# Kernel tuning notes

Measured on AMD Instinct MI355X. Metric: run time of the kernel, lower is better.

The kernel has to match this reference:

```python
import jax, jax.numpy as jnp
import numpy as np

# SREChead (single level, width=0.25): stem 1x1 (128->64) + two 3x3 convs (64->64),
# each Conv->BN(eval, folded into scale/shift)->SiLU, then 1x1 reg (4ch) and obj (1ch)
# heads, followed by YOLOX-style grid decode.
B, C_IN, HGT, WID = 64, 128, 80, 80
C_H = 64            # int(256 * 0.25)
STRIDE = 32


def _conv(x, w):
    # NCHW conv, stride 1, SAME padding (pad=(k-1)//2 as in BaseConv)
    return jax.lax.conv_general_dilated(
        x, w, window_strides=(1, 1), padding='SAME',
        dimension_numbers=('NCHW', 'OIHW', 'NCHW'))


def _bn_silu(y, scale, shift):
    # eval-mode BatchNorm folded to per-channel affine, then SiLU
    return jax.nn.silu(y * scale[None, :, None, None] + shift[None, :, None, None])


def setup_inputs() -> dict:
    key = jax.random.key(0)
    ks = jax.random.split(key, 12)

    def w(k, o, i, kh, kw, s=0.05):
        return jax.random.normal(k, (o, i, kh, kw), jnp.float32) * s

    def bn(k, c):
        k1, k2 = jax.random.split(k)
        scale = 1.0 + 0.1 * jax.random.normal(k1, (c,), jnp.float32)
        shift = 0.05 * jax.random.normal(k2, (c,), jnp.float32)
        return scale, shift

    stem_scale, stem_shift = bn(ks[2], C_H)
    c1_scale, c1_shift = bn(ks[4], C_H)
    c2_scale, c2_shift = bn(ks[6], C_H)
    return {
        'x': jax.random.normal(ks[0], (B, C_IN, HGT, WID), jnp.float32),
        'stem_w': w(ks[1], C_H, C_IN, 1, 1),
        'stem_scale': stem_scale, 'stem_shift': stem_shift,
        'c1_w': w(ks[3], C_H, C_H, 3, 3),
        'c1_scale': c1_scale, 'c1_shift': c1_shift,
        'c2_w': w(ks[5], C_H, C_H, 3, 3),
        'c2_scale': c2_scale, 'c2_shift': c2_shift,
        'reg_w': w(ks[7], 4, C_H, 1, 1),
        'reg_b': jnp.zeros((4,), jnp.float32),
        'obj_w': w(ks[8], 1, C_H, 1, 1),
        'obj_b': jnp.zeros((1,), jnp.float32),
    }


def reference(x, stem_w, stem_scale, stem_shift,
              c1_w, c1_scale, c1_shift,
              c2_w, c2_scale, c2_shift,
              reg_w, reg_b, obj_w, obj_b):
    f = _bn_silu(_conv(x, stem_w), stem_scale, stem_shift)       # [B,64,H,W]
    f = _bn_silu(_conv(f, c1_w), c1_scale, c1_shift)
    f = _bn_silu(_conv(f, c2_w), c2_scale, c2_shift)
    reg = _conv(f, reg_w) + reg_b[None, :, None, None]           # [B,4,H,W]
    obj = jax.nn.sigmoid(_conv(f, obj_w) + obj_b[None, :, None, None])  # [B,1,H,W]
    out = jnp.concatenate([reg, obj], axis=1)                    # [B,5,H,W]
    out = out.reshape(out.shape[0], 5, HGT * WID).transpose(0, 2, 1)  # [B,HW,5]
    # YOLOX decode: xy = (pred_xy + grid) * stride, wh = exp(pred_wh) * stride
    yv, xv = jnp.meshgrid(jnp.arange(HGT), jnp.arange(WID), indexing='ij')
    grid = jnp.stack([xv, yv], -1).reshape(1, HGT * WID, 2).astype(out.dtype)
    xy = (out[..., :2] + grid) * STRIDE
    wh = jnp.exp(out[..., 2:4]) * STRIDE
    return jnp.concatenate([xy, wh, out[..., 4:5]], axis=-1)     # [B,HW,5]
```

## Files before the change

### kernel.cpp

```cpp
#include <hip/hip_runtime.h>
#include <cstdint>


typedef short short8 __attribute__((ext_vector_type(8)));
typedef float floatx4 __attribute__((ext_vector_type(4)));
typedef float fx4 __attribute__((ext_vector_type(4)));
typedef unsigned short us4 __attribute__((ext_vector_type(4)));

#define NPIX 6400
#define CGS  3952
#define CGS2 2576

static __device__ __forceinline__ unsigned short f2bf(float f) {
    unsigned u = __builtin_bit_cast(unsigned, f);
    u += 0x7fffu + ((u >> 16) & 1u);
    return (unsigned short)(u >> 16);
}

static __device__ __forceinline__ float silu_(float v) {
    return v / (1.0f + __expf(-v));
}

__global__ __launch_bounds__(256) void rearr_w_kernel(
    const float* __restrict__ ws_, const float* __restrict__ w1,
    const float* __restrict__ w2,
    unsigned short* __restrict__ wS, unsigned short* __restrict__ wB1,
    unsigned short* __restrict__ wB2) {
    int idx = blockIdx.x * 256 + threadIdx.x;
    if (idx < 8192) {
        int e = idx;
        int j = e & 7, lane = (e >> 3) & 63, ct = (e >> 9) & 3, kb = e >> 11;
        int co = ct * 16 + (lane & 15);
        int ci = kb * 32 + ((lane >> 4) * 8) + j;
        wS[e] = f2bf(ws_[co * 128 + ci]);
        return;
    }
    idx -= 8192;
    const float* src = (idx < 36864) ? w1 : w2;
    unsigned short* dst = (idx < 36864) ? wB1 : wB2;
    int e = (idx < 36864) ? idx : idx - 36864;
    int j = e & 7, lane = (e >> 3) & 63, ct = (e >> 9) & 3, kb = e >> 11;
    int co = ct * 16 + (lane & 15);
    int k = kb * 32 + ((lane >> 4) * 8) + j;
    int ci = k & 63, tap = k >> 6;
    dst[e] = f2bf(src[(co * 64 + ci) * 9 + tap]);
}

__global__ __launch_bounds__(256) void stem_kernel(
    const float* __restrict__ x, const unsigned short* __restrict__ wS,
    const float* __restrict__ scale, const float* __restrict__ shift,
    unsigned short* __restrict__ f1) {
    __shared__ __align__(16) float xs[64 * 129];
    int b = blockIdx.y;
    int tid = threadIdx.x;
    int pbase = blockIdx.x * 128;
    int lane = tid & 63, wv = tid >> 6;
    int l15 = lane & 15, q = lane >> 4;

    float sc[4][4], sh[4][4];
    #pragma unroll
    for (int ct = 0; ct < 4; ++ct)
        #pragma unroll
        for (int r = 0; r < 4; ++r) {
            sc[ct][r] = scale[ct * 16 + q * 4 + r];
            sh[ct][r] = shift[ct * 16 + q * 4 + r];
        }

    floatx4 acc[4][2];
    floatx4 zf = {0.0f, 0.0f, 0.0f, 0.0f};
    #pragma unroll
    for (int ct = 0; ct < 4; ++ct)
        #pragma unroll
        for (int t = 0; t < 2; ++t) acc[ct][t] = zf;

    #pragma unroll
    for (int p = 0; p < 2; ++p) {
        if (p) __syncthreads();
        #pragma unroll
        for (int i = 0; i < 8; ++i) {
            int c = i * 256 + tid;
            int row = c >> 5, seg = c & 31;
            fx4 v = *(const fx4*)(
                x + ((size_t)(b * 128 + p * 64 + row)) * NPIX + pbase + seg * 4);
            *(fx4*)(xs + row * 129 + seg * 4) = v;
        }
        __syncthreads();

        #pragma unroll
        for (int kk = 0; kk < 2; ++kk) {
            int kb = p * 2 + kk;
            short8 wf[4];
            #pragma unroll
            for (int ct = 0; ct < 4; ++ct)
                wf[ct] = *(const short8*)(wS + ((kb * 4 + ct) * 64 + lane) * 8);
            short8 xf[2];
            #pragma unroll
            for (int t = 0; t < 2; ++t) {
                int px = (wv * 2 + t) * 16 + l15;
                const float* src = xs + (kk * 32 + q * 8) * 129 + px;
                unsigned short tmp[8];
                #pragma unroll
                for (int j = 0; j < 8; ++j) tmp[j] = f2bf(src[j * 129]);
                xf[t] = *(const short8*)tmp;
            }
            #pragma unroll
            for (int ct = 0; ct < 4; ++ct)
                #pragma unroll
                for (int t = 0; t < 2; ++t)
                    acc[ct][t] = __builtin_amdgcn_mfma_f32_16x16x32_bf16(
                        wf[ct], xf[t], acc[ct][t], 0, 0, 0);
        }
    }

    #pragma unroll
    for (int t = 0; t < 2; ++t) {
        int pg = pbase + (wv * 2 + t) * 16 + l15;
        unsigned short* dst = f1 + ((size_t)b * NPIX + pg) * 64;
        #pragma unroll
        for (int ct = 0; ct < 4; ++ct) {
            us4 v;
            #pragma unroll
            for (int r = 0; r < 4; ++r)
                v[r] = f2bf(silu_(acc[ct][t][r] * sc[ct][r] + sh[ct][r]));
            *(us4*)(dst + ct * 16 + q * 4) = v;
        }
    }
}

static __device__ __forceinline__ void conv_core(
    const unsigned short* __restrict__ fin, const unsigned short* __restrict__ wB,
    unsigned short* tile, floatx4 (*acc)[5], int b, int y0,
    int tid, int lane, int wv, int l15, int q) {
    const unsigned short* fb = fin + (size_t)b * NPIX * 64;
    floatx4 zf = {0.0f, 0.0f, 0.0f, 0.0f};
    #pragma unroll
    for (int c4 = 0; c4 < 4; ++c4)
        #pragma unroll
        for (int pt = 0; pt < 5; ++pt) acc[c4][pt] = zf;

    #pragma unroll
    for (int half = 0; half < 2; ++half) {
        if (half) __syncthreads();
        #pragma unroll
        for (int i = 0; i < 8; ++i) {
            int cid = i * 256 + tid;
            if (cid < 1968) {
                int pixL = cid >> 2, g = cid & 3;
                int r = pixL / 82, c = pixL - r * 82;
                int gy = y0 - 1 + r, gx = c - 1;
                short8 v = {};
                if ((unsigned)gy < 80u && (unsigned)gx < 80u)
                    v = *(const short8*)(
                        fb + (size_t)(gy * 80 + gx) * 64 + half * 32 + g * 8);
                *(short8*)(tile + g * CGS + pixL * 8) = v;
            }
        }
        __syncthreads();

        #pragma unroll
        for (int trow = 0; trow < 3; ++trow) {
            const int dy = trow - 1;
            #pragma unroll
            for (int tc = 0; tc < 3; ++tc) {
                const int dx = tc - 1;
                const int kb = (trow * 3 + tc) * 2 + half;
                short8 w4[4];
                #pragma unroll
                for (int c4 = 0; c4 < 4; ++c4)
                    w4[c4] = *(const short8*)(wB + ((kb * 4 + c4) * 64 + lane) * 8);
                #pragma unroll
                for (int pt = 0; pt < 5; ++pt) {
                    int pix = (wv + 1 + dy) * 82 + pt * 16 + l15 + 1 + dx;
                    short8 b8 = *(const short8*)(tile + q * CGS + pix * 8);
                    #pragma unroll
                    for (int c4 = 0; c4 < 4; ++c4)
                        acc[c4][pt] = __builtin_amdgcn_mfma_f32_16x16x32_bf16(
                            w4[c4], b8, acc[c4][pt], 0, 0, 0);
                }
            }
        }
    }
}

__global__ __launch_bounds__(256, 3) void conv3_kernel(
    const unsigned short* __restrict__ fin, const unsigned short* __restrict__ wB,
    const float* __restrict__ scale, const float* __restrict__ shift,
    unsigned short* __restrict__ fout) {
    __shared__ __align__(16) unsigned short tile[8 * CGS2];
    int b = blockIdx.y, y0 = blockIdx.x * 4;
    int tid = threadIdx.x;
    int lane = tid & 63, wv = tid >> 6;
    int l15 = lane & 15, q = lane >> 4;

    floatx4 acc[4][5];
    conv_core(fin, wB, tile, acc, b, y0, tid, lane, wv, l15, q);

    float sc4[4][4], sh4[4][4];
    #pragma unroll
    for (int c4 = 0; c4 < 4; ++c4)
        #pragma unroll
        for (int r = 0; r < 4; ++r) {
            sc4[c4][r] = scale[c4 * 16 + q * 4 + r];
            sh4[c4][r] = shift[c4 * 16 + q * 4 + r];
        }
    #pragma unroll
    for (int pt = 0; pt < 5; ++pt) {
        int pg = (y0 + wv) * 80 + pt * 16 + l15;
        unsigned short* dst = fout + ((size_t)b * NPIX + pg) * 64;
        #pragma unroll
        for (int c4 = 0; c4 < 4; ++c4) {
            us4 v;
            #pragma unroll
            for (int r = 0; r < 4; ++r)
                v[r] = f2bf(silu_(acc[c4][pt][r] * sc4[c4][r] + sh4[c4][r]));
            *(us4*)(dst + c4 * 16 + q * 4) = v;
        }
    }
}

__global__ __launch_bounds__(256, 3) void conv_head_kernel(
    const unsigned short* __restrict__ fin, const unsigned short* __restrict__ wB,
    const float* __restrict__ scale, const float* __restrict__ shift,
    const float* __restrict__ reg_w, const float* __restrict__ reg_b,
    const float* __restrict__ obj_w, const float* __restrict__ obj_b,
    float* __restrict__ out) {
    __shared__ __align__(16) unsigned short tile[8 * CGS2];
    int b = blockIdx.y, y0 = blockIdx.x * 4;
    int tid = threadIdx.x;
    int lane = tid & 63, wv = tid >> 6;
    int l15 = lane & 15, q = lane >> 4;

    floatx4 acc[4][5];
    conv_core(fin, wB, tile, acc, b, y0, tid, lane, wv, l15, q);

    __syncthreads();

    float sc4[4][4], sh4[4][4];
    #pragma unroll
    for (int c4 = 0; c4 < 4; ++c4)
        #pragma unroll
        for (int r = 0; r < 4; ++r) {
            sc4[c4][r] = scale[c4 * 16 + q * 4 + r];
            sh4[c4][r] = shift[c4 * 16 + q * 4 + r];
        }
    #pragma unroll
    for (int pt = 0; pt < 5; ++pt) {
        int pix = wv * 80 + pt * 16 + l15;
        #pragma unroll
        for (int c4 = 0; c4 < 4; ++c4) {
            int gco = c4 * 2 + (q >> 1);
            us4 v;
            #pragma unroll
            for (int r = 0; r < 4; ++r)
                v[r] = f2bf(silu_(acc[c4][pt][r] * sc4[c4][r] + sh4[c4][r]));
            *(us4*)(tile + gco * CGS2 + pix * 8 + (q & 1) * 4) = v;
        }
    }

    short8 hbf[2];
    #pragma unroll
    for (int kb2 = 0; kb2 < 2; ++kb2) {
        int k0 = kb2 * 32 + q * 8;
        short8 f = {};
        if (l15 < 4) {
            #pragma unroll
            for (int j = 0; j < 8; ++j) f[j] = (short)f2bf(reg_w[l15 * 64 + k0 + j]);
        } else if (l15 == 4) {
            #pragma unroll
            for (int j = 0; j < 8; ++j) f[j] = (short)f2bf(obj_w[k0 + j]);
        }
        hbf[kb2] = f;
    }

    __syncthreads();

    floatx4 zf = {0.0f, 0.0f, 0.0f, 0.0f};
    floatx4 acc5[5];
    #pragma unroll
    for (int t = 0; t < 5; ++t) acc5[t] = zf;
    #pragma unroll
    for (int t = 0; t < 5; ++t) {
        int mt = wv * 5 + t;
        int pix = mt * 16 + l15;
        #pragma unroll
        for (int kb2 = 0; kb2 < 2; ++kb2) {
            short8 a = *(const short8*)(tile + (kb2 * 4 + q) * CGS2 + pix * 8);
            acc5[t] = __builtin_amdgcn_mfma_f32_16x16x32_bf16(
                a, hbf[kb2], acc5[t], 0, 0, 0);
        }
    }

    float bias = 0.0f;
    if (l15 < 4) bias = reg_b[l15];
    else if (l15 == 4) bias = obj_b[0];

    #pragma unroll
    for (int t = 0; t < 5; ++t) {
        int mt = wv * 5 + t;
        #pragma unroll
        for (int r = 0; r < 4; ++r) {
            int pixL = mt * 16 + q * 4 + r;
            if (l15 < 5) {
                float v = acc5[t][r] + bias;
                float gx = (float)(pixL % 80);
                float gy = (float)(y0 + pixL / 80);
                float o;
                if (l15 == 0)      o = (v + gx) * 32.0f;
                else if (l15 == 1) o = (v + gy) * 32.0f;
                else if (l15 < 4)  o = __expf(v) * 32.0f;
                else               o = 1.0f / (1.0f + __expf(-v));
                out[((size_t)b * NPIX + y0 * 80 + pixL) * 5 + l15] = o;
            }
        }
    }
}

extern "C" void kernel_launch(void* const* d_in, const int* in_sizes, int n_in,
                              void* d_out, int out_size, void* d_ws, size_t ws_size,
                              hipStream_t stream) {
    const float* x          = (const float*)d_in[0];
    const float* stem_w     = (const float*)d_in[1];
    const float* stem_scale = (const float*)d_in[2];
    const float* stem_shift = (const float*)d_in[3];
    const float* c1_w       = (const float*)d_in[4];
    const float* c1_scale   = (const float*)d_in[5];
    const float* c1_shift   = (const float*)d_in[6];
    const float* c2_w       = (const float*)d_in[7];
    const float* c2_scale   = (const float*)d_in[8];
    const float* c2_shift   = (const float*)d_in[9];
    const float* reg_w      = (const float*)d_in[10];
    const float* reg_b      = (const float*)d_in[11];
    const float* obj_w      = (const float*)d_in[12];
    const float* obj_b      = (const float*)d_in[13];
    float* out = (float*)d_out;

    const size_t needed = ((size_t)8192 + 73728 + 2 * (size_t)64 * NPIX * 64) * 2;
    if (ws_size < needed) return;

    unsigned short* ws  = (unsigned short*)d_ws;
    unsigned short* wS  = ws;
    unsigned short* wB1 = ws + 8192;
    unsigned short* wB2 = wB1 + 36864;
    unsigned short* f1  = wB2 + 36864;
    unsigned short* f2  = f1 + (size_t)64 * NPIX * 64;

    rearr_w_kernel<<<320, 256, 0, stream>>>(stem_w, c1_w, c2_w, wS, wB1, wB2);
    stem_kernel<<<dim3(50, 64), 256, 0, stream>>>(x, wS, stem_scale, stem_shift, f1);
    conv3_kernel<<<dim3(20, 64), 256, 0, stream>>>(f1, wB1, c1_scale, c1_shift, f2);
    conv_head_kernel<<<dim3(20, 64), 256, 0, stream>>>(f2, wB2, c2_scale, c2_shift,
                                                       reg_w, reg_b, obj_w, obj_b, out);
}
```

Baseline: 443.4 us.

## Load full 64-channel halo tile via direct global-to-LDS loads in one pass

```diff
diff --git a/kernel.cpp b/kernel.cpp
--- a/kernel.cpp
+++ b/kernel.cpp
@@ -8,7 +8,7 @@
 typedef unsigned short us4 __attribute__((ext_vector_type(4)));
 
 #define NPIX 6400
-#define CGS  3952
+#define SEGP 4112
 #define CGS2 2576
 
 static __device__ __forceinline__ unsigned short f2bf(float f) {
@@ -21,11 +21,18 @@
     return v / (1.0f + __expf(-v));
 }
 
+static __device__ __forceinline__ void gload_lds16(const void* g, void* l) {
+    __builtin_amdgcn_global_load_lds(
+        (const __attribute__((address_space(1))) unsigned int*)g,
+        (__attribute__((address_space(3))) unsigned int*)l, 16, 0, 0);
+}
+
 __global__ __launch_bounds__(256) void rearr_w_kernel(
     const float* __restrict__ ws_, const float* __restrict__ w1,
     const float* __restrict__ w2,
     unsigned short* __restrict__ wS, unsigned short* __restrict__ wB1,
-    unsigned short* __restrict__ wB2) {
+    unsigned short* __restrict__ wB2, unsigned short* __restrict__ zb) {
+    if (blockIdx.x == 0 && threadIdx.x < 16) zb[threadIdx.x] = 0;
     int idx = blockIdx.x * 256 + threadIdx.x;
     if (idx < 8192) {
         int e = idx;
@@ -129,6 +136,7 @@
 
 static __device__ __forceinline__ void conv_core(
     const unsigned short* __restrict__ fin, const unsigned short* __restrict__ wB,
+    const unsigned short* __restrict__ zbuf,
     unsigned short* tile, floatx4 (*acc)[5], int b, int y0,
     int tid, int lane, int wv, int l15, int q) {
     const unsigned short* fb = fin + (size_t)b * NPIX * 64;
@@ -139,30 +147,30 @@
         for (int pt = 0; pt < 5; ++pt) acc[c4][pt] = zf;
 
     #pragma unroll
-    for (int half = 0; half < 2; ++half) {
-        if (half) __syncthreads();
-        #pragma unroll
-        for (int i = 0; i < 8; ++i) {
-            int cid = i * 256 + tid;
-            if (cid < 1968) {
-                int pixL = cid >> 2, g = cid & 3;
-                int r = pixL / 82, c = pixL - r * 82;
-                int gy = y0 - 1 + r, gx = c - 1;
-                short8 v = {};
-                if ((unsigned)gy < 80u && (unsigned)gx < 80u)
-                    v = *(const short8*)(
-                        fb + (size_t)(gy * 80 + gx) * 64 + half * 32 + g * 8);
-                *(short8*)(tile + g * CGS + pixL * 8) = v;
-            }
-        }
-        __syncthreads();
-
-        #pragma unroll
-        for (int trow = 0; trow < 3; ++trow) {
-            const int dy = trow - 1;
-            #pragma unroll
-            for (int tc = 0; tc < 3; ++tc) {
-                const int dx = tc - 1;
+    for (int i = 0; i < 16; ++i) {
+        int cbase = i * 256 + wv * 64;
+        int g = cbase >> 9;
+        int pixB = cbase & 511;
+        int pixL = pixB + lane;
+        int r = (pixL * 25) >> 11;
+        int c = pixL - r * 82;
+        int gy = y0 - 1 + r, gx = c - 1;
+        const unsigned short* src =
+            (pixL < 492 && (unsigned)gy < 80u && (unsigned)gx < 80u)
+                ? fb + (size_t)(gy * 80 + gx) * 64 + g * 8
+                : zbuf;
+        gload_lds16(src, tile + (size_t)g * SEGP + (size_t)pixB * 8);
+    }
+    __syncthreads();
+
+    #pragma unroll
+    for (int trow = 0; trow < 3; ++trow) {
+        const int dy = trow - 1;
+        #pragma unroll
+        for (int tc = 0; tc < 3; ++tc) {
+            const int dx = tc - 1;
+            #pragma unroll
+            for (int half = 0; half < 2; ++half) {
                 const int kb = (trow * 3 + tc) * 2 + half;
                 short8 w4[4];
                 #pragma unroll
@@ -171,7 +179,8 @@
                 #pragma unroll
                 for (int pt = 0; pt < 5; ++pt) {
                     int pix = (wv + 1 + dy) * 82 + pt * 16 + l15 + 1 + dx;
-                    short8 b8 = *(const short8*)(tile + q * CGS + pix * 8);
+                    short8 b8 = *(const short8*)(
+                        tile + (size_t)(half * 4 + q) * SEGP + pix * 8);
                     #pragma unroll
                     for (int c4 = 0; c4 < 4; ++c4)
                         acc[c4][pt] = __builtin_amdgcn_mfma_f32_16x16x32_bf16(
@@ -182,18 +191,19 @@
     }
 }
 
-__global__ __launch_bounds__(256, 3) void conv3_kernel(
+__global__ __launch_bounds__(256, 2) void conv3_kernel(
     const unsigned short* __restrict__ fin, const unsigned short* __restrict__ wB,
+    const unsigned short* __restrict__ zbuf,
     const float* __restrict__ scale, const float* __restrict__ shift,
     unsigned short* __restrict__ fout) {
-    __shared__ __align__(16) unsigned short tile[8 * CGS2];
+    __shared__ __align__(16) unsigned short tile[8 * SEGP];
     int b = blockIdx.y, y0 = blockIdx.x * 4;
     int tid = threadIdx.x;
     int lane = tid & 63, wv = tid >> 6;
     int l15 = lane & 15, q = lane >> 4;
 
     floatx4 acc[4][5];
-    conv_core(fin, wB, tile, acc, b, y0, tid, lane, wv, l15, q);
+    conv_core(fin, wB, zbuf, tile, acc, b, y0, tid, lane, wv, l15, q);
 
     float sc4[4][4], sh4[4][4];
     #pragma unroll
@@ -218,20 +228,21 @@
     }
 }
 
-__global__ __launch_bounds__(256, 3) void conv_head_kernel(
+__global__ __launch_bounds__(256, 2) void conv_head_kernel(
     const unsigned short* __restrict__ fin, const unsigned short* __restrict__ wB,
+    const unsigned short* __restrict__ zbuf,
     const float* __restrict__ scale, const float* __restrict__ shift,
     const float* __restrict__ reg_w, const float* __restrict__ reg_b,
     const float* __restrict__ obj_w, const float* __restrict__ obj_b,
     float* __restrict__ out) {
-    __shared__ __align__(16) unsigned short tile[8 * CGS2];
+    __shared__ __align__(16) unsigned short tile[8 * SEGP];
     int b = blockIdx.y, y0 = blockIdx.x * 4;
     int tid = threadIdx.x;
     int lane = tid & 63, wv = tid >> 6;
     int l15 = lane & 15, q = lane >> 4;
 
     floatx4 acc[4][5];
-    conv_core(fin, wB, tile, acc, b, y0, tid, lane, wv, l15, q);
+    conv_core(fin, wB, zbuf, tile, acc, b, y0, tid, lane, wv, l15, q);
 
     __syncthreads();
 
@@ -334,7 +345,8 @@
     const float* obj_b      = (const float*)d_in[13];
     float* out = (float*)d_out;
 
-    const size_t needed = ((size_t)8192 + 73728 + 2 * (size_t)64 * NPIX * 64) * 2;
+    const size_t needed =
+        ((size_t)8192 + 73728 + 2 * (size_t)64 * NPIX * 64 + 16) * 2;
     if (ws_size < needed) return;
 
     unsigned short* ws  = (unsigned short*)d_ws;
@@ -343,10 +355,11 @@
     unsigned short* wB2 = wB1 + 36864;
     unsigned short* f1  = wB2 + 36864;
     unsigned short* f2  = f1 + (size_t)64 * NPIX * 64;
-
-    rearr_w_kernel<<<320, 256, 0, stream>>>(stem_w, c1_w, c2_w, wS, wB1, wB2);
+    unsigned short* zb  = f2 + (size_t)64 * NPIX * 64;
+
+    rearr_w_kernel<<<320, 256, 0, stream>>>(stem_w, c1_w, c2_w, wS, wB1, wB2, zb);
     stem_kernel<<<dim3(50, 64), 256, 0, stream>>>(x, wS, stem_scale, stem_shift, f1);
-    conv3_kernel<<<dim3(20, 64), 256, 0, stream>>>(f1, wB1, c1_scale, c1_shift, f2);
-    conv_head_kernel<<<dim3(20, 64), 256, 0, stream>>>(f2, wB2, c2_scale, c2_shift,
+    conv3_kernel<<<dim3(20, 64), 256, 0, stream>>>(f1, wB1, zb, c1_scale, c1_shift, f2);
+    conv_head_kernel<<<dim3(20, 64), 256, 0, stream>>>(f2, wB2, zb, c2_scale, c2_shift,
                                                        reg_w, reg_b, obj_w, obj_b, out);
 }
```

Result: slower. 458.1 us (+3.3%).
